# Kernel tuning notes

Measured on AMD Instinct MI355X. Metric: run time of the kernel, lower is better.

Reference implementation:

```python
import jax, jax.numpy as jnp
import numpy as np

DEPTH = 4
HEADS = 8
WINDOW = 256
RPW = 2                      # relay_tokens_per_window
SEQ_PER_RELAY = WINDOW // RPW  # 128 tokens per relay group
RELAY_START = 2              # depth_start_relay_attn (1-indexed layer number)
LN_EPS = 1e-5


def setup_inputs() -> dict:
    key = jax.random.key(0)
    ks = jax.random.split(key, 8)
    b, t, d, dff = 2, 2048, 512, 2048
    s = 0.02
    return {
        "x": jax.random.normal(ks[0], (b, t, d), dtype=jnp.float32),
        "relay_emb": jax.random.normal(ks[1], (1, d), dtype=jnp.float32) * s,
        "ln1_g": jnp.ones((DEPTH, d), jnp.float32),
        "ln1_b": jnp.zeros((DEPTH, d), jnp.float32),
        "loc_qkv_w": jax.random.normal(ks[2], (DEPTH, d, 3 * d), dtype=jnp.float32) * s,
        "loc_out_w": jax.random.normal(ks[3], (DEPTH, d, d), dtype=jnp.float32) * s,
        "loc_out_b": jnp.zeros((DEPTH, d), jnp.float32),
        "glob_qkv_w": jax.random.normal(ks[4], (DEPTH, d, 3 * d), dtype=jnp.float32) * s,
        "glob_out_w": jax.random.normal(ks[5], (DEPTH, d, d), dtype=jnp.float32) * s,
        "glob_out_b": jnp.zeros((DEPTH, d), jnp.float32),
        "ln2_g": jnp.ones((DEPTH, d), jnp.float32),
        "ln2_b": jnp.zeros((DEPTH, d), jnp.float32),
        "ff_w1": jax.random.normal(ks[6], (DEPTH, d, dff), dtype=jnp.float32) * s,
        "ff_b1": jnp.zeros((DEPTH, dff), jnp.float32),
        "ff_w2": jax.random.normal(ks[7], (DEPTH, dff, d), dtype=jnp.float32) * s,
        "ff_b2": jnp.zeros((DEPTH, d), jnp.float32),
    }


def _layernorm(x, g, b):
    m = jnp.mean(x, axis=-1, keepdims=True)
    v = jnp.mean(jnp.square(x - m), axis=-1, keepdims=True)
    return (x - m) * jax.lax.rsqrt(v + LN_EPS) * g + b


def _self_attention(x, qkv_w, out_w, out_b):
    # full (non-causal) multi-head attention, as in FullAttention
    b, t, d = x.shape
    h, dh = HEADS, d // HEADS
    q, k, v = jnp.split(x @ qkv_w, 3, axis=-1)
    mh = lambda u: u.reshape(b, t, h, dh).transpose(0, 2, 1, 3)  # b h t dh
    q, k, v = mh(q), mh(k), mh(v)
    dots = jnp.einsum('bhid,bhjd->bhij', q, k) * (dh ** -0.5)
    attn = jax.nn.softmax(dots, axis=-1)
    o = jnp.einsum('bhij,bhjd->bhid', attn, v)
    o = o.transpose(0, 2, 1, 3).reshape(b, t, d)
    return o @ out_w + out_b


def reference(x, relay_emb, ln1_g, ln1_b, loc_qkv_w, loc_out_w, loc_out_b,
              glob_qkv_w, glob_out_w, glob_out_b, ln2_g, ln2_b,
              ff_w1, ff_b1, ff_w2, ff_b2):
    b, t, d = x.shape
    # insert one relay token every SEQ_PER_RELAY tokens
    x = x.reshape(b, -1, SEQ_PER_RELAY, d)
    G = x.shape[1]
    rel = jnp.broadcast_to(relay_emb[None, None], (b, G, 1, d))
    x = jnp.concatenate([rel, x], axis=2).reshape(b, -1, d)  # (b, G*(129), d)

    for l in range(DEPTH):
        # attention block: PreNorm -> AttentionLayer, residual from sequence wrapper
        y = _layernorm(x, ln1_g[l], ln1_b[l])
        if (l + 1) >= RELAY_START:
            y = y.reshape(b, G, SEQ_PER_RELAY + 1, d)
            r = y[:, :, 0]                                       # (b, G, d) relay tokens
            r = _self_attention(r, glob_qkv_w[l], glob_out_w[l], glob_out_b[l]) + r
            y = jnp.concatenate([r[:, :, None], y[:, :, 1:]], axis=2).reshape(b, -1, d)
        x = x + _self_attention(y, loc_qkv_w[l], loc_out_w[l], loc_out_b[l])
        # feedforward block: PreNorm -> FFN with LeakyReLU(0.01)
        z = _layernorm(x, ln2_g[l], ln2_b[l])
        z = jax.nn.leaky_relu(z @ ff_w1[l] + ff_b1[l], negative_slope=0.01) @ ff_w2[l] + ff_b2[l]
        x = x + z

    # strip relay tokens
    x = x.reshape(b, G, SEQ_PER_RELAY + 1, d)
    return x[:, :, 1:].reshape(b, -1, d)
```

## Files before the change

kernel.cpp:

```cpp
#include <hip/hip_runtime.h>

typedef __attribute__((ext_vector_type(8))) __bf16 bf16x8;
typedef __attribute__((ext_vector_type(8))) unsigned short u16x8;
typedef __attribute__((ext_vector_type(4))) unsigned short u16x4;
typedef __attribute__((ext_vector_type(4))) float f32x4;
typedef unsigned short u16;

#define TSEQ 2064
#define NTOK 4128
#define MPAD 4224

__device__ __forceinline__ float bf2f(u16 u) {
  unsigned x = ((unsigned)u) << 16;
  return __builtin_bit_cast(float, x);
}
__device__ __forceinline__ u16 f2bf(float f) {
  unsigned u = __builtin_bit_cast(unsigned, f);
  u += 0x7fffu + ((u >> 16) & 1u);
  return (u16)(u >> 16);
}

__device__ __forceinline__ void gll16(const u16* g, u16* l) {
  __builtin_amdgcn_global_load_lds((const __attribute__((address_space(1))) void*)g,
                                   (__attribute__((address_space(3))) void*)l, 16, 0, 0);
}
__device__ __forceinline__ int swz(int row, int col) {
  return row * 64 + (col ^ ((row & 7) << 3));
}

__global__ __launch_bounds__(256) void transpose_w(const float* __restrict__ src,
                                                   u16* __restrict__ dst,
                                                   int K, int N)
{
  __shared__ float tile[32][33];
  const int l = blockIdx.z;
  src += (size_t)l * K * N;
  dst += (size_t)l * K * N;
  const int n0 = blockIdx.x * 32, k0 = blockIdx.y * 32;
  const int c = threadIdx.x & 31, r = threadIdx.x >> 5;
#pragma unroll
  for (int rr = r; rr < 32; rr += 8)
    tile[rr][c] = src[(size_t)(k0 + rr) * N + n0 + c];
  __syncthreads();
#pragma unroll
  for (int rr = r; rr < 32; rr += 8)
    dst[(size_t)(n0 + rr) * K + k0 + c] = f2bf(tile[c][rr]);
}

__global__ void build_x(const float* __restrict__ xin, const float* __restrict__ relay,
                        float* __restrict__ xw)
{
  const int total = 2 * TSEQ * 512;
  for (int idx = blockIdx.x * 256 + threadIdx.x; idx < total; idx += gridDim.x * 256) {
    int col = idx & 511;
    int tok = (idx >> 9) % TSEQ;
    int b   = idx / (TSEQ * 512);
    int g = tok / 129, s = tok % 129;
    float v = (s == 0) ? relay[col]
                       : xin[((size_t)b * 2048 + g * 128 + (s - 1)) * 512 + col];
    xw[idx] = v;
  }
}

__global__ void extract_out(const float* __restrict__ xw, float* __restrict__ out)
{
  const int total = 2 * 2048 * 512;
  for (int idx = blockIdx.x * 256 + threadIdx.x; idx < total; idx += gridDim.x * 256) {
    int col = idx & 511;
    int tok = (idx >> 9) & 2047;
    int b   = idx / (2048 * 512);
    int g = tok >> 7, s = tok & 127;
    out[idx] = xw[((size_t)b * TSEQ + g * 129 + s + 1) * 512 + col];
  }
}

__global__ __launch_bounds__(256) void ln_kernel(const float* __restrict__ x,
                                                 const float* __restrict__ g,
                                                 const float* __restrict__ bta,
                                                 u16* __restrict__ y, int M)
{
  const int wid = threadIdx.x >> 6, lane = threadIdx.x & 63;
  const int row = blockIdx.x * 4 + wid;
  if (row >= M) return;
  const float* xr = x + (size_t)row * 512;
  float v[8];
  float s = 0.f;
#pragma unroll
  for (int j = 0; j < 8; ++j) { v[j] = xr[j * 64 + lane]; s += v[j]; }
#pragma unroll
  for (int m = 1; m <= 32; m <<= 1) s += __shfl_xor(s, m);
  float mean = s * (1.f / 512.f);
  float vs = 0.f;
#pragma unroll
  for (int j = 0; j < 8; ++j) { float d = v[j] - mean; vs += d * d; }
#pragma unroll
  for (int m = 1; m <= 32; m <<= 1) vs += __shfl_xor(vs, m);
  float rstd = rsqrtf(vs * (1.f / 512.f) + 1e-5f);
  u16* yr = y + (size_t)row * 512;
#pragma unroll
  for (int j = 0; j < 8; ++j) {
    int c = j * 64 + lane;
    yr[c] = f2bf((v[j] - mean) * rstd * g[c] + bta[c]);
  }
}

template<bool HAS_BIAS, bool ACT, bool RESID, bool OUT_BF16, bool VOUT>
__global__ __launch_bounds__(256) void gemm2(
    const u16* __restrict__ A, const u16* __restrict__ Bt,
    const float* __restrict__ bias, const float* __restrict__ resid,
    void* __restrict__ outp, u16* __restrict__ vgout, int M, int N, int K)
{
  __shared__ __attribute__((aligned(16))) u16 As[2][128 * 64];
  __shared__ __attribute__((aligned(16))) u16 Bs[2][128 * 64];
  const int tid = threadIdx.x, lane = tid & 63, wid = tid >> 6;
  const int row0 = blockIdx.x * 128, col0 = blockIdx.y * 128;
  const int wm = (wid >> 1) * 64, wn = (wid & 1) * 64;
  const int srow = tid >> 3, sseg = tid & 7;
  f32x4 acc[4][4];
#pragma unroll
  for (int m = 0; m < 4; ++m)
#pragma unroll
    for (int n = 0; n < 4; ++n) acc[m][n] = (f32x4)0.f;
  const u16* Ab = A + (size_t)row0 * K;
  const u16* Bb = Bt + (size_t)col0 * K;
#pragma unroll
  for (int i = 0; i < 4; ++i) {
    int row = srow + i * 32, ss = sseg ^ (row & 7);
    gll16(Ab + (size_t)row * K + ss * 8, &As[0][row * 64 + sseg * 8]);
    gll16(Bb + (size_t)row * K + ss * 8, &Bs[0][row * 64 + sseg * 8]);
  }
  const int fr = lane & 15, g = lane >> 4;
  int cur = 0;
  for (int k0 = 0; k0 < K; k0 += 64) {
    __syncthreads();
    if (k0 + 64 < K) {
      u16* ad = &As[cur ^ 1][0];
      u16* bd = &Bs[cur ^ 1][0];
#pragma unroll
      for (int i = 0; i < 4; ++i) {
        int row = srow + i * 32, ss = sseg ^ (row & 7);
        gll16(Ab + (size_t)row * K + k0 + 64 + ss * 8, ad + row * 64 + sseg * 8);
        gll16(Bb + (size_t)row * K + k0 + 64 + ss * 8, bd + row * 64 + sseg * 8);
      }
    }
    const u16* as_ = &As[cur][0];
    const u16* bs_ = &Bs[cur][0];
    bf16x8 a[2][4], bb[2][4];
#pragma unroll
    for (int kk = 0; kk < 2; ++kk) {
#pragma unroll
      for (int m = 0; m < 4; ++m) a[kk][m] = *(const bf16x8*)&as_[swz(wm + m * 16 + fr, kk * 32 + g * 8)];
#pragma unroll
      for (int n = 0; n < 4; ++n) bb[kk][n] = *(const bf16x8*)&bs_[swz(wn + n * 16 + fr, kk * 32 + g * 8)];
    }
    __builtin_amdgcn_s_setprio(1);
#pragma unroll
    for (int kk = 0; kk < 2; ++kk)
#pragma unroll
      for (int m = 0; m < 4; ++m)
#pragma unroll
        for (int n = 0; n < 4; ++n)
          acc[m][n] = __builtin_amdgcn_mfma_f32_16x16x32_bf16(a[kk][m], bb[kk][n], acc[m][n], 0, 0, 0);
    __builtin_amdgcn_s_setprio(0);
    cur ^= 1;
  }

#pragma unroll
  for (int m = 0; m < 4; ++m) {
#pragma unroll
    for (int n = 0; n < 4; ++n) {
#pragma unroll
      for (int j = 0; j < 4; ++j) {
        int grow = row0 + wm + m * 16 + g * 4 + j;
        int gcol = col0 + wn + n * 16 + fr;
        if (grow < M) {
          float v = acc[m][n][j];
          if (HAS_BIAS) v += bias[gcol];
          if (ACT) v = (v > 0.f) ? v : 0.01f * v;
          if (RESID) v += resid[(size_t)grow * N + gcol];
          if (VOUT && gcol >= 1024) {
            int hh = (gcol - 1024) >> 6, dd = gcol & 63;
            int bb2 = grow >= TSEQ;
            int tok = grow - bb2 * TSEQ;
            vgout[((size_t)((bb2 * 8 + hh) * 64 + dd)) * 2112 + tok] = f2bf(v);
          } else if (OUT_BF16) {
            ((u16*)outp)[(size_t)grow * N + gcol] = f2bf(v);
          } else {
            ((float*)outp)[(size_t)grow * N + gcol] = v;
          }
        }
      }
    }
  }
}

__global__ __launch_bounds__(256) void flash_attn3(const u16* __restrict__ big,
                                                   const u16* __restrict__ vg,
                                                   u16* __restrict__ op0,
                                                   u16* __restrict__ op1,
                                                   float2* __restrict__ mlb)
{
  __shared__ __attribute__((aligned(16))) u16 Qs[64 * 64];
  __shared__ __attribute__((aligned(16))) u16 Ks[2][64 * 64];
  __shared__ __attribute__((aligned(16))) u16 Vs[2][64 * 64];
  const int tid = threadIdx.x, lane = tid & 63, wid = tid >> 6;
  const int qt = blockIdx.x, bh = blockIdx.y, z = blockIdx.z;
  const int b = bh >> 3, h = bh & 7;
  const int q0 = qt * 64;
  const int srow = tid >> 3, sseg = tid & 7;
  const int ktbeg = z * 17, ktend = z ? 33 : 17;

  const u16* qb = big + ((size_t)(b * TSEQ) + q0) * 1536 + h * 64;
  const u16* kb = big + ((size_t)(b * TSEQ)) * 1536 + h * 64 + 512;
  const u16* vb = vg + (size_t)bh * 64 * 2112;
#pragma unroll
  for (int i = 0; i < 2; ++i) {
    int row = srow + i * 32, ss = sseg ^ (row & 7);
    gll16(qb + (size_t)row * 1536 + ss * 8, &Qs[row * 64 + sseg * 8]);
    gll16(kb + (size_t)(ktbeg * 64 + row) * 1536 + ss * 8, &Ks[0][row * 64 + sseg * 8]);
    gll16(vb + (size_t)row * 2112 + ktbeg * 64 + ss * 8, &Vs[0][row * 64 + sseg * 8]);
  }
  __syncthreads();
  const int fr = lane & 15, g = lane >> 4;
  bf16x8 aq0 = *(const bf16x8*)&Qs[swz(wid * 16 + fr, g * 8)];
  bf16x8 aq1 = *(const bf16x8*)&Qs[swz(wid * 16 + fr, 32 + g * 8)];
  u16* Pw = &Qs[wid * 1024];

  f32x4 oacc[4];
#pragma unroll
  for (int nf = 0; nf < 4; ++nf) oacc[nf] = (f32x4)0.f;
  float mrow = -1e30f, lsum = 0.f;
  int cur = 0;

  for (int kt = ktbeg; kt < ktend; ++kt) {
    if (kt + 1 < ktend) {
      const u16* kb2 = kb + (size_t)(kt + 1) * 64 * 1536;
      const u16* vb2 = vb + (kt + 1) * 64;
      u16* kd = &Ks[cur ^ 1][0];
      u16* vd = &Vs[cur ^ 1][0];
#pragma unroll
      for (int i = 0; i < 2; ++i) {
        int row = srow + i * 32, ss = sseg ^ (row & 7);
        gll16(kb2 + (size_t)row * 1536 + ss * 8, kd + row * 64 + sseg * 8);
        gll16(vb2 + (size_t)row * 2112 + ss * 8, vd + row * 64 + sseg * 8);
      }
    }
    const u16* ks = &Ks[cur][0];
    const u16* vs = &Vs[cur][0];
    f32x4 s[4];
    __builtin_amdgcn_s_setprio(1);
#pragma unroll
    for (int n = 0; n < 4; ++n) {
      int row = n * 16 + fr;
      bf16x8 ak0 = *(const bf16x8*)&ks[swz(row, g * 8)];
      bf16x8 ak1 = *(const bf16x8*)&ks[swz(row, 32 + g * 8)];
      f32x4 t = (f32x4)0.f;
      t = __builtin_amdgcn_mfma_f32_16x16x32_bf16(ak0, aq0, t, 0, 0, 0);
      t = __builtin_amdgcn_mfma_f32_16x16x32_bf16(ak1, aq1, t, 0, 0, 0);
      s[n] = t;
    }
    __builtin_amdgcn_s_setprio(0);
#pragma unroll
    for (int n = 0; n < 4; ++n) {
      int kbase = kt * 64 + n * 16 + g * 4;
#pragma unroll
      for (int j = 0; j < 4; ++j)
        s[n][j] = (kbase + j < TSEQ) ? s[n][j] * 0.125f : -1e30f;
    }
    float mloc = s[0][0];
#pragma unroll
    for (int n = 0; n < 4; ++n)
#pragma unroll
      for (int j = 0; j < 4; ++j) mloc = fmaxf(mloc, s[n][j]);
    mloc = fmaxf(mloc, __shfl_xor(mloc, 16));
    mloc = fmaxf(mloc, __shfl_xor(mloc, 32));
    float nm = fmaxf(mrow, mloc);
    float sc = __expf(mrow - nm);
    mrow = nm;
    lsum *= sc;
    float psum = 0.f;
#pragma unroll
    for (int n = 0; n < 4; ++n) {
      u16x4 pw;
#pragma unroll
      for (int j = 0; j < 4; ++j) {
        float p = __expf(s[n][j] - nm);
        psum += p;
        pw[j] = f2bf(p);
      }
      *(u16x4*)&Pw[swz(fr, n * 16 + g * 4)] = pw;
    }
    psum += __shfl_xor(psum, 16);
    psum += __shfl_xor(psum, 32);
    lsum += psum;
    float s4[4];
#pragma unroll
    for (int j = 0; j < 4; ++j) s4[j] = __shfl(sc, g * 4 + j);
#pragma unroll
    for (int nf = 0; nf < 4; ++nf)
#pragma unroll
      for (int j = 0; j < 4; ++j) oacc[nf][j] *= s4[j];
    __builtin_amdgcn_s_setprio(1);
#pragma unroll
    for (int kc = 0; kc < 2; ++kc) {
      bf16x8 ap = *(const bf16x8*)&Pw[swz(fr, kc * 32 + g * 8)];
#pragma unroll
      for (int nf = 0; nf < 4; ++nf) {
        bf16x8 bv = *(const bf16x8*)&vs[swz(nf * 16 + fr, kc * 32 + g * 8)];
        oacc[nf] = __builtin_amdgcn_mfma_f32_16x16x32_bf16(ap, bv, oacc[nf], 0, 0, 0);
      }
    }
    __builtin_amdgcn_s_setprio(0);
    __syncthreads();
    cur ^= 1;
  }

  u16* op = z ? op1 : op0;
#pragma unroll
  for (int nf = 0; nf < 4; ++nf) {
#pragma unroll
    for (int j = 0; j < 4; ++j) {
      int row = q0 + wid * 16 + g * 4 + j;
      if (row < TSEQ)
        op[((size_t)(b * TSEQ + row)) * 512 + h * 64 + nf * 16 + fr] = f2bf(oacc[nf][j]);
    }
  }
  if (lane < 16) {
    int row = q0 + wid * 16 + fr;
    if (row < TSEQ)
      mlb[(size_t)(z * 16 + bh) * 2112 + row] = float2{mrow, lsum};
  }
}

__global__ __launch_bounds__(256) void fa_combine(const u16* __restrict__ op0,
                                                  const u16* __restrict__ op1,
                                                  const float2* __restrict__ mlb,
                                                  u16* __restrict__ ob)
{
  int idx = blockIdx.x * 256 + threadIdx.x;
  int tok = idx >> 7;
  int c4 = (idx & 127) * 4;
  int b = tok >= TSEQ;
  int row = tok - b * TSEQ;
  int h = c4 >> 6;
  float2 ml0 = mlb[(size_t)(b * 8 + h) * 2112 + row];
  float2 ml1 = mlb[(size_t)(16 + b * 8 + h) * 2112 + row];
  float M = fmaxf(ml0.x, ml1.x);
  float a0 = __expf(ml0.x - M), a1 = __expf(ml1.x - M);
  float inv = 1.f / (ml0.y * a0 + ml1.y * a1);
  u16x4 v0 = *(const u16x4*)&op0[(size_t)tok * 512 + c4];
  u16x4 v1 = *(const u16x4*)&op1[(size_t)tok * 512 + c4];
  u16x4 o;
#pragma unroll
  for (int j = 0; j < 4; ++j)
    o[j] = f2bf((bf2f(v0[j]) * a0 + bf2f(v1[j]) * a1) * inv);
  *(u16x4*)&ob[(size_t)tok * 512 + c4] = o;
}

__global__ __launch_bounds__(256) void global_attn(const u16* __restrict__ rqkv,
                                                   u16* __restrict__ ro)
{
  const int b = blockIdx.x >> 3, h = blockIdx.x & 7;
  __shared__ float q[16][64], k[16][64], v[16][64], s[16][16], p[16][16];
  const int tid = threadIdx.x;
  for (int idx = tid; idx < 1024; idx += 256) {
    int rr = idx >> 6, c = idx & 63;
    size_t base = (size_t)(b * 16 + rr) * 1536 + h * 64 + c;
    q[rr][c] = bf2f(rqkv[base]);
    k[rr][c] = bf2f(rqkv[base + 512]);
    v[rr][c] = bf2f(rqkv[base + 1024]);
  }
  __syncthreads();
  {
    int i = tid >> 4, j = tid & 15;
    float acc = 0.f;
#pragma unroll
    for (int d = 0; d < 64; ++d) acc += q[i][d] * k[j][d];
    s[i][j] = acc * 0.125f;
  }
  __syncthreads();
  if (tid < 16) {
    float mx = -1e30f;
#pragma unroll
    for (int j = 0; j < 16; ++j) mx = fmaxf(mx, s[tid][j]);
    float sum = 0.f;
#pragma unroll
    for (int j = 0; j < 16; ++j) { float e = __expf(s[tid][j] - mx); p[tid][j] = e; sum += e; }
    float iv = 1.f / sum;
#pragma unroll
    for (int j = 0; j < 16; ++j) p[tid][j] *= iv;
  }
  __syncthreads();
  for (int idx = tid; idx < 1024; idx += 256) {
    int rr = idx >> 6, c = idx & 63;
    float acc = 0.f;
#pragma unroll
    for (int j = 0; j < 16; ++j) acc += p[rr][j] * v[j][c];
    ro[(size_t)(b * 16 + rr) * 512 + h * 64 + c] = f2bf(acc);
  }
}

__global__ void gather_relay(const u16* __restrict__ y, u16* __restrict__ rbuf)
{
  int idx = blockIdx.x * 256 + threadIdx.x;
  int col = idx & 511, rr = idx >> 9;
  int b = rr >> 4, g = rr & 15;
  rbuf[idx] = y[((size_t)b * TSEQ + g * 129) * 512 + col];
}

__global__ void relay_scatter(const float* __restrict__ rout, const u16* __restrict__ rbuf,
                              u16* __restrict__ y)
{
  int idx = blockIdx.x * 256 + threadIdx.x;
  int col = idx & 511, rr = idx >> 9;
  int b = rr >> 4, g = rr & 15;
  y[((size_t)b * TSEQ + g * 129) * 512 + col] = f2bf(rout[idx] + bf2f(rbuf[idx]));
}

extern "C" void kernel_launch(void* const* d_in, const int* in_sizes, int n_in,
                              void* d_out, int out_size, void* d_ws, size_t ws_size,
                              hipStream_t stream)
{
  const float* x_in     = (const float*)d_in[0];
  const float* rel_emb  = (const float*)d_in[1];
  const float* ln1_g    = (const float*)d_in[2];
  const float* ln1_b    = (const float*)d_in[3];
  const float* loc_qkv  = (const float*)d_in[4];
  const float* loc_ow   = (const float*)d_in[5];
  const float* loc_ob   = (const float*)d_in[6];
  const float* glob_qkv = (const float*)d_in[7];
  const float* glob_ow  = (const float*)d_in[8];
  const float* glob_ob  = (const float*)d_in[9];
  const float* ln2_g    = (const float*)d_in[10];
  const float* ln2_b    = (const float*)d_in[11];
  const float* ff_w1    = (const float*)d_in[12];
  const float* ff_b1    = (const float*)d_in[13];
  const float* ff_w2    = (const float*)d_in[14];
  const float* ff_b2    = (const float*)d_in[15];

  char* ws = (char*)d_ws;
  float* xbuf = (float*)(ws + 0);
  u16*   ybuf = (u16*)(ws + 8650752);
  u16*   obuf = (u16*)(ws + 12976128);
  u16*   big  = (u16*)(ws + 17301504);
  u16*   vg   = (u16*)(ws + 34603008);
  u16*   wLQ  = (u16*)(ws + 38928384);
  u16*   wGQ  = (u16*)(ws + 45219840);
  u16*   wLO  = (u16*)(ws + 51511296);
  u16*   wGO  = (u16*)(ws + 53608448);
  u16*   wF1  = (u16*)(ws + 55705600);
  u16*   wF2  = (u16*)(ws + 64094208);
  u16*   rbuf = (u16*)(ws + 72482816);
  u16*   rqkv = (u16*)(ws + 72613888);
  u16*   rov  = (u16*)(ws + 72712192);
  float* rout = (float*)(ws + 72843264);
  float2* mlb = (float2*)(ws + 72908800);

  dim3 B(256);
  transpose_w<<<dim3(48, 16, 4), B, 0, stream>>>(loc_qkv, wLQ, 512, 1536);
  transpose_w<<<dim3(48, 16, 4), B, 0, stream>>>(glob_qkv, wGQ, 512, 1536);
  transpose_w<<<dim3(16, 16, 4), B, 0, stream>>>(loc_ow, wLO, 512, 512);
  transpose_w<<<dim3(16, 16, 4), B, 0, stream>>>(glob_ow, wGO, 512, 512);
  transpose_w<<<dim3(64, 16, 4), B, 0, stream>>>(ff_w1, wF1, 512, 2048);
  transpose_w<<<dim3(16, 64, 4), B, 0, stream>>>(ff_w2, wF2, 2048, 512);

  build_x<<<8256, B, 0, stream>>>(x_in, rel_emb, xbuf);

  for (int l = 0; l < 4; ++l) {
    ln_kernel<<<1032, B, 0, stream>>>(xbuf, ln1_g + l * 512, ln1_b + l * 512, ybuf, NTOK);
    if (l + 1 >= 2) {
      gather_relay<<<64, B, 0, stream>>>(ybuf, rbuf);
      gemm2<false, false, false, true, false><<<dim3(1, 12), B, 0, stream>>>(
          rbuf, wGQ + (size_t)l * 1536 * 512, nullptr, nullptr, rqkv, nullptr, 32, 1536, 512);
      global_attn<<<16, B, 0, stream>>>(rqkv, rov);
      gemm2<true, false, false, false, false><<<dim3(1, 4), B, 0, stream>>>(
          rov, wGO + (size_t)l * 512 * 512, glob_ob + l * 512, nullptr, rout, nullptr, 32, 512, 512);
      relay_scatter<<<64, B, 0, stream>>>(rout, rbuf, ybuf);
    }
    gemm2<false, false, false, true, true><<<dim3(33, 12), B, 0, stream>>>(
        ybuf, wLQ + (size_t)l * 1536 * 512, nullptr, nullptr, big, vg, NTOK, 1536, 512);
    flash_attn3<<<dim3(33, 16, 2), B, 0, stream>>>(big, vg, ybuf, obuf, mlb);
    fa_combine<<<2064, B, 0, stream>>>(ybuf, obuf, mlb, obuf);
    gemm2<true, false, true, false, false><<<dim3(33, 4), B, 0, stream>>>(
        obuf, wLO + (size_t)l * 512 * 512, loc_ob + l * 512, xbuf, xbuf, nullptr, NTOK, 512, 512);
    ln_kernel<<<1032, B, 0, stream>>>(xbuf, ln2_g + l * 512, ln2_b + l * 512, ybuf, NTOK);
    gemm2<true, true, false, true, false><<<dim3(33, 16), B, 0, stream>>>(
        ybuf, wF1 + (size_t)l * 2048 * 512, ff_b1 + l * 2048, nullptr, big, nullptr, NTOK, 2048, 512);
    gemm2<true, false, true, false, false><<<dim3(33, 4), B, 0, stream>>>(
        big, wF2 + (size_t)l * 512 * 2048, ff_b2 + l * 512, xbuf, xbuf, nullptr, NTOK, 512, 2048);
  }
  extract_out<<<8192, B, 0, stream>>>(xbuf, (float*)d_out);
}
```

Measured before the change: 1.071 ms.

## Fuse relay gather/scatter into GEMM, single-buffer GEMM, 128-row flash attention with lazy rescale

The six weight-transpose launches are merged into one kernel, and the relay gather/scatter kernels are folded into the GEMM's A-row indexing and epilogue. The GEMM drops double-buffered LDS for a single buffer with an occupancy hint, which trades load/compute overlap for more resident blocks. Flash attention now uses 512-thread blocks covering 128 query rows. The softmax scale is pre-applied to Q in the QKV GEMM epilogue, masking runs only on the last tile, and the running-max rescale is skipped while the max stays within a threshold. P is packed to bf16 by truncation rather than round-to-nearest, which slightly changes numerics.

```diff
diff --git a/kernel.cpp b/kernel.cpp
--- a/kernel.cpp
+++ b/kernel.cpp
@@ -3,12 +3,13 @@
 typedef __attribute__((ext_vector_type(8))) __bf16 bf16x8;
 typedef __attribute__((ext_vector_type(8))) unsigned short u16x8;
 typedef __attribute__((ext_vector_type(4))) unsigned short u16x4;
+typedef __attribute__((ext_vector_type(2))) unsigned int u32x2;
 typedef __attribute__((ext_vector_type(4))) float f32x4;
 typedef unsigned short u16;
+typedef unsigned int u32;
 
 #define TSEQ 2064
 #define NTOK 4128
-#define MPAD 4224
 
 __device__ __forceinline__ float bf2f(u16 u) {
   unsigned x = ((unsigned)u) << 16;
@@ -28,22 +29,34 @@
   return row * 64 + (col ^ ((row & 7) << 3));
 }
 
-__global__ __launch_bounds__(256) void transpose_w(const float* __restrict__ src,
-                                                   u16* __restrict__ dst,
-                                                   int K, int N)
+__global__ __launch_bounds__(256) void transpose_all(
+    const float* __restrict__ s0, const float* __restrict__ s1,
+    const float* __restrict__ s2, const float* __restrict__ s3,
+    const float* __restrict__ s4, const float* __restrict__ s5,
+    u16* __restrict__ d0, u16* __restrict__ d1, u16* __restrict__ d2,
+    u16* __restrict__ d3, u16* __restrict__ d4, u16* __restrict__ d5)
 {
   __shared__ float tile[32][33];
-  const int l = blockIdx.z;
+  int bid = blockIdx.x;
+  const float* src; u16* dst; int K, N, r;
+  if (bid < 6144)       { int w = bid >> 11 >= 1 && bid >= 3072; r = bid - (bid >= 3072 ? 3072 : 0);
+                          K = 512; N = 1536; src = bid >= 3072 ? s1 : s0; dst = bid >= 3072 ? d1 : d0; }
+  else if (bid < 8192)  { r = bid - (bid >= 7168 ? 7168 : 6144);
+                          K = 512; N = 512;  src = bid >= 7168 ? s3 : s2; dst = bid >= 7168 ? d3 : d2; }
+  else if (bid < 12288) { r = bid - 8192;  K = 512;  N = 2048; src = s4; dst = d4; }
+  else                  { r = bid - 12288; K = 2048; N = 512;  src = s5; dst = d5; }
+  const int tx = N >> 5, per = tx * (K >> 5);
+  const int l = r / per; r -= l * per;
+  const int n0 = (r % tx) * 32, k0 = (r / tx) * 32;
   src += (size_t)l * K * N;
   dst += (size_t)l * K * N;
-  const int n0 = blockIdx.x * 32, k0 = blockIdx.y * 32;
-  const int c = threadIdx.x & 31, r = threadIdx.x >> 5;
-#pragma unroll
-  for (int rr = r; rr < 32; rr += 8)
+  const int c = threadIdx.x & 31, rr0 = threadIdx.x >> 5;
+#pragma unroll
+  for (int rr = rr0; rr < 32; rr += 8)
     tile[rr][c] = src[(size_t)(k0 + rr) * N + n0 + c];
   __syncthreads();
 #pragma unroll
-  for (int rr = r; rr < 32; rr += 8)
+  for (int rr = rr0; rr < 32; rr += 8)
     dst[(size_t)(n0 + rr) * K + k0 + c] = f2bf(tile[c][rr]);
 }
 
@@ -104,14 +117,19 @@
   }
 }
 
-template<bool HAS_BIAS, bool ACT, bool RESID, bool OUT_BF16, bool VOUT>
-__global__ __launch_bounds__(256) void gemm2(
+__device__ __forceinline__ int relay_tok(int r) {
+  return (r >> 4) * TSEQ + (r & 15) * 129;
+}
+
+template<bool HAS_BIAS, bool ACT, bool RESID, bool OUT_BF16, bool VOUT,
+         bool RELAYA, bool RELAYC>
+__global__ __launch_bounds__(256, 4) void gemm3(
     const u16* __restrict__ A, const u16* __restrict__ Bt,
     const float* __restrict__ bias, const float* __restrict__ resid,
     void* __restrict__ outp, u16* __restrict__ vgout, int M, int N, int K)
 {
-  __shared__ __attribute__((aligned(16))) u16 As[2][128 * 64];
-  __shared__ __attribute__((aligned(16))) u16 Bs[2][128 * 64];
+  __shared__ __attribute__((aligned(16))) u16 As[128 * 64];
+  __shared__ __attribute__((aligned(16))) u16 Bs[128 * 64];
   const int tid = threadIdx.x, lane = tid & 63, wid = tid >> 6;
   const int row0 = blockIdx.x * 128, col0 = blockIdx.y * 128;
   const int wm = (wid >> 1) * 64, wn = (wid & 1) * 64;
@@ -121,48 +139,34 @@
   for (int m = 0; m < 4; ++m)
 #pragma unroll
     for (int n = 0; n < 4; ++n) acc[m][n] = (f32x4)0.f;
-  const u16* Ab = A + (size_t)row0 * K;
   const u16* Bb = Bt + (size_t)col0 * K;
-#pragma unroll
-  for (int i = 0; i < 4; ++i) {
-    int row = srow + i * 32, ss = sseg ^ (row & 7);
-    gll16(Ab + (size_t)row * K + ss * 8, &As[0][row * 64 + sseg * 8]);
-    gll16(Bb + (size_t)row * K + ss * 8, &Bs[0][row * 64 + sseg * 8]);
-  }
   const int fr = lane & 15, g = lane >> 4;
-  int cur = 0;
+
   for (int k0 = 0; k0 < K; k0 += 64) {
     __syncthreads();
-    if (k0 + 64 < K) {
-      u16* ad = &As[cur ^ 1][0];
-      u16* bd = &Bs[cur ^ 1][0];
-#pragma unroll
-      for (int i = 0; i < 4; ++i) {
-        int row = srow + i * 32, ss = sseg ^ (row & 7);
-        gll16(Ab + (size_t)row * K + k0 + 64 + ss * 8, ad + row * 64 + sseg * 8);
-        gll16(Bb + (size_t)row * K + k0 + 64 + ss * 8, bd + row * 64 + sseg * 8);
-      }
-    }
-    const u16* as_ = &As[cur][0];
-    const u16* bs_ = &Bs[cur][0];
-    bf16x8 a[2][4], bb[2][4];
+#pragma unroll
+    for (int i = 0; i < 4; ++i) {
+      int row = srow + i * 32, ss = sseg ^ (row & 7);
+      size_t arow = RELAYA ? (size_t)relay_tok(row & 31) : (size_t)(row0 + row);
+      gll16(A + arow * K + k0 + ss * 8, &As[row * 64 + sseg * 8]);
+      gll16(Bb + (size_t)row * K + k0 + ss * 8, &Bs[row * 64 + sseg * 8]);
+    }
+    __syncthreads();
 #pragma unroll
     for (int kk = 0; kk < 2; ++kk) {
-#pragma unroll
-      for (int m = 0; m < 4; ++m) a[kk][m] = *(const bf16x8*)&as_[swz(wm + m * 16 + fr, kk * 32 + g * 8)];
-#pragma unroll
-      for (int n = 0; n < 4; ++n) bb[kk][n] = *(const bf16x8*)&bs_[swz(wn + n * 16 + fr, kk * 32 + g * 8)];
-    }
-    __builtin_amdgcn_s_setprio(1);
-#pragma unroll
-    for (int kk = 0; kk < 2; ++kk)
+      bf16x8 a[4], bb[4];
+#pragma unroll
+      for (int m = 0; m < 4; ++m) a[m] = *(const bf16x8*)&As[swz(wm + m * 16 + fr, kk * 32 + g * 8)];
+#pragma unroll
+      for (int n = 0; n < 4; ++n) bb[n] = *(const bf16x8*)&Bs[swz(wn + n * 16 + fr, kk * 32 + g * 8)];
+      __builtin_amdgcn_s_setprio(1);
 #pragma unroll
       for (int m = 0; m < 4; ++m)
 #pragma unroll
         for (int n = 0; n < 4; ++n)
-          acc[m][n] = __builtin_amdgcn_mfma_f32_16x16x32_bf16(a[kk][m], bb[kk][n], acc[m][n], 0, 0, 0);
-    __builtin_amdgcn_s_setprio(0);
-    cur ^= 1;
+          acc[m][n] = __builtin_amdgcn_mfma_f32_16x16x32_bf16(a[m], bb[n], acc[m][n], 0, 0, 0);
+      __builtin_amdgcn_s_setprio(0);
+    }
   }
 
 #pragma unroll
@@ -178,12 +182,16 @@
           if (HAS_BIAS) v += bias[gcol];
           if (ACT) v = (v > 0.f) ? v : 0.01f * v;
           if (RESID) v += resid[(size_t)grow * N + gcol];
-          if (VOUT && gcol >= 1024) {
+          if (RELAYC) {
+            u16* p = (u16*)outp + (size_t)relay_tok(grow) * 512 + gcol;
+            *p = f2bf(v + bf2f(*p));
+          } else if (VOUT && gcol >= 1024) {
             int hh = (gcol - 1024) >> 6, dd = gcol & 63;
             int bb2 = grow >= TSEQ;
             int tok = grow - bb2 * TSEQ;
             vgout[((size_t)((bb2 * 8 + hh) * 64 + dd)) * 2112 + tok] = f2bf(v);
           } else if (OUT_BF16) {
+            if (VOUT && gcol < 512) v *= 0.125f;
             ((u16*)outp)[(size_t)grow * N + gcol] = f2bf(v);
           } else {
             ((float*)outp)[(size_t)grow * N + gcol] = v;
@@ -194,31 +202,35 @@
   }
 }
 
-__global__ __launch_bounds__(256) void flash_attn3(const u16* __restrict__ big,
-                                                   const u16* __restrict__ vg,
-                                                   u16* __restrict__ op0,
-                                                   u16* __restrict__ op1,
-                                                   float2* __restrict__ mlb)
-{
-  __shared__ __attribute__((aligned(16))) u16 Qs[64 * 64];
+__global__ __launch_bounds__(512, 4) void flash_attn4(const u16* __restrict__ big,
+                                                      const u16* __restrict__ vg,
+                                                      u16* __restrict__ op0,
+                                                      u16* __restrict__ op1,
+                                                      float2* __restrict__ mlb)
+{
+  __shared__ __attribute__((aligned(16))) u16 Qs[128 * 64];
   __shared__ __attribute__((aligned(16))) u16 Ks[2][64 * 64];
   __shared__ __attribute__((aligned(16))) u16 Vs[2][64 * 64];
   const int tid = threadIdx.x, lane = tid & 63, wid = tid >> 6;
   const int qt = blockIdx.x, bh = blockIdx.y, z = blockIdx.z;
   const int b = bh >> 3, h = bh & 7;
-  const int q0 = qt * 64;
+  const int q0 = qt * 128;
   const int srow = tid >> 3, sseg = tid & 7;
   const int ktbeg = z * 17, ktend = z ? 33 : 17;
 
-  const u16* qb = big + ((size_t)(b * TSEQ) + q0) * 1536 + h * 64;
   const u16* kb = big + ((size_t)(b * TSEQ)) * 1536 + h * 64 + 512;
   const u16* vb = vg + (size_t)bh * 64 * 2112;
 #pragma unroll
   for (int i = 0; i < 2; ++i) {
-    int row = srow + i * 32, ss = sseg ^ (row & 7);
-    gll16(qb + (size_t)row * 1536 + ss * 8, &Qs[row * 64 + sseg * 8]);
-    gll16(kb + (size_t)(ktbeg * 64 + row) * 1536 + ss * 8, &Ks[0][row * 64 + sseg * 8]);
-    gll16(vb + (size_t)row * 2112 + ktbeg * 64 + ss * 8, &Vs[0][row * 64 + sseg * 8]);
+    int row = srow + i * 64;
+    int grow = b * TSEQ + q0 + row; grow = grow < NTOK ? grow : NTOK - 1;
+    int ss = sseg ^ (row & 7);
+    gll16(big + (size_t)grow * 1536 + h * 64 + ss * 8, &Qs[row * 64 + sseg * 8]);
+  }
+  {
+    int ss = sseg ^ (srow & 7);
+    gll16(kb + (size_t)(ktbeg * 64 + srow) * 1536 + ss * 8, &Ks[0][srow * 64 + sseg * 8]);
+    gll16(vb + (size_t)srow * 2112 + ktbeg * 64 + ss * 8, &Vs[0][srow * 64 + sseg * 8]);
   }
   __syncthreads();
   const int fr = lane & 15, g = lane >> 4;
@@ -234,16 +246,9 @@
 
   for (int kt = ktbeg; kt < ktend; ++kt) {
     if (kt + 1 < ktend) {
-      const u16* kb2 = kb + (size_t)(kt + 1) * 64 * 1536;
-      const u16* vb2 = vb + (kt + 1) * 64;
-      u16* kd = &Ks[cur ^ 1][0];
-      u16* vd = &Vs[cur ^ 1][0];
-#pragma unroll
-      for (int i = 0; i < 2; ++i) {
-        int row = srow + i * 32, ss = sseg ^ (row & 7);
-        gll16(kb2 + (size_t)row * 1536 + ss * 8, kd + row * 64 + sseg * 8);
-        gll16(vb2 + (size_t)row * 2112 + ss * 8, vd + row * 64 + sseg * 8);
-      }
+      int ss = sseg ^ (srow & 7);
+      gll16(kb + (size_t)((kt + 1) * 64 + srow) * 1536 + ss * 8, &Ks[cur ^ 1][srow * 64 + sseg * 8]);
+      gll16(vb + (size_t)srow * 2112 + (kt + 1) * 64 + ss * 8, &Vs[cur ^ 1][srow * 64 + sseg * 8]);
     }
     const u16* ks = &Ks[cur][0];
     const u16* vs = &Vs[cur][0];
@@ -260,12 +265,14 @@
       s[n] = t;
     }
     __builtin_amdgcn_s_setprio(0);
-#pragma unroll
-    for (int n = 0; n < 4; ++n) {
-      int kbase = kt * 64 + n * 16 + g * 4;
-#pragma unroll
-      for (int j = 0; j < 4; ++j)
-        s[n][j] = (kbase + j < TSEQ) ? s[n][j] * 0.125f : -1e30f;
+    if (kt == 32) {
+#pragma unroll
+      for (int n = 0; n < 4; ++n) {
+        int kbase = kt * 64 + n * 16 + g * 4;
+#pragma unroll
+        for (int j = 0; j < 4; ++j)
+          if (kbase + j >= TSEQ) s[n][j] = -1e30f;
+      }
     }
     float mloc = s[0][0];
 #pragma unroll
@@ -274,32 +281,33 @@
       for (int j = 0; j < 4; ++j) mloc = fmaxf(mloc, s[n][j]);
     mloc = fmaxf(mloc, __shfl_xor(mloc, 16));
     mloc = fmaxf(mloc, __shfl_xor(mloc, 32));
-    float nm = fmaxf(mrow, mloc);
-    float sc = __expf(mrow - nm);
-    mrow = nm;
-    lsum *= sc;
+    if (!__all(mloc <= mrow + 8.f)) {
+      float nm = fmaxf(mrow, mloc);
+      float sc = __expf(mrow - nm);
+      mrow = nm;
+      lsum *= sc;
+      float s4[4];
+#pragma unroll
+      for (int j = 0; j < 4; ++j) s4[j] = __shfl(sc, g * 4 + j);
+#pragma unroll
+      for (int nf = 0; nf < 4; ++nf)
+#pragma unroll
+        for (int j = 0; j < 4; ++j) oacc[nf][j] *= s4[j];
+    }
     float psum = 0.f;
 #pragma unroll
     for (int n = 0; n < 4; ++n) {
-      u16x4 pw;
-#pragma unroll
-      for (int j = 0; j < 4; ++j) {
-        float p = __expf(s[n][j] - nm);
-        psum += p;
-        pw[j] = f2bf(p);
-      }
-      *(u16x4*)&Pw[swz(fr, n * 16 + g * 4)] = pw;
+      float p0 = __expf(s[n][0] - mrow), p1 = __expf(s[n][1] - mrow);
+      float p2 = __expf(s[n][2] - mrow), p3 = __expf(s[n][3] - mrow);
+      psum += (p0 + p1) + (p2 + p3);
+      u32x2 pk;
+      pk[0] = __builtin_amdgcn_perm(__builtin_bit_cast(u32, p1), __builtin_bit_cast(u32, p0), 0x07060302u);
+      pk[1] = __builtin_amdgcn_perm(__builtin_bit_cast(u32, p3), __builtin_bit_cast(u32, p2), 0x07060302u);
+      *(u32x2*)&Pw[swz(fr, n * 16 + g * 4)] = pk;
     }
     psum += __shfl_xor(psum, 16);
     psum += __shfl_xor(psum, 32);
     lsum += psum;
-    float s4[4];
-#pragma unroll
-    for (int j = 0; j < 4; ++j) s4[j] = __shfl(sc, g * 4 + j);
-#pragma unroll
-    for (int nf = 0; nf < 4; ++nf)
-#pragma unroll
-      for (int j = 0; j < 4; ++j) oacc[nf][j] *= s4[j];
     __builtin_amdgcn_s_setprio(1);
 #pragma unroll
     for (int kc = 0; kc < 2; ++kc) {
@@ -398,23 +406,6 @@
     for (int j = 0; j < 16; ++j) acc += p[rr][j] * v[j][c];
     ro[(size_t)(b * 16 + rr) * 512 + h * 64 + c] = f2bf(acc);
   }
-}
-
-__global__ void gather_relay(const u16* __restrict__ y, u16* __restrict__ rbuf)
-{
-  int idx = blockIdx.x * 256 + threadIdx.x;
-  int col = idx & 511, rr = idx >> 9;
-  int b = rr >> 4, g = rr & 15;
-  rbuf[idx] = y[((size_t)b * TSEQ + g * 129) * 512 + col];
-}
-
-__global__ void relay_scatter(const float* __restrict__ rout, const u16* __restrict__ rbuf,
-                              u16* __restrict__ y)
-{
-  int idx = blockIdx.x * 256 + threadIdx.x;
-  int col = idx & 511, rr = idx >> 9;
-  int b = rr >> 4, g = rr & 15;
-  y[((size_t)b * TSEQ + g * 129) * 512 + col] = f2bf(rout[idx] + bf2f(rbuf[idx]));
 }
 
 extern "C" void kernel_launch(void* const* d_in, const int* in_sizes, int n_in,
@@ -439,54 +430,45 @@
   const float* ff_b2    = (const float*)d_in[15];
 
   char* ws = (char*)d_ws;
-  float* xbuf = (float*)(ws + 0);
-  u16*   ybuf = (u16*)(ws + 8650752);
-  u16*   obuf = (u16*)(ws + 12976128);
-  u16*   big  = (u16*)(ws + 17301504);
-  u16*   vg   = (u16*)(ws + 34603008);
-  u16*   wLQ  = (u16*)(ws + 38928384);
-  u16*   wGQ  = (u16*)(ws + 45219840);
-  u16*   wLO  = (u16*)(ws + 51511296);
-  u16*   wGO  = (u16*)(ws + 53608448);
-  u16*   wF1  = (u16*)(ws + 55705600);
-  u16*   wF2  = (u16*)(ws + 64094208);
-  u16*   rbuf = (u16*)(ws + 72482816);
-  u16*   rqkv = (u16*)(ws + 72613888);
-  u16*   rov  = (u16*)(ws + 72712192);
-  float* rout = (float*)(ws + 72843264);
-  float2* mlb = (float2*)(ws + 72908800);
+  float*  xbuf = (float*)(ws + 0);
+  u16*    ybuf = (u16*)(ws + 8650752);
+  u16*    obuf = (u16*)(ws + 12976128);
+  u16*    big  = (u16*)(ws + 17301504);
+  u16*    vg   = (u16*)(ws + 34603008);
+  u16*    wLQ  = (u16*)(ws + 38928384);
+  u16*    wGQ  = (u16*)(ws + 45219840);
+  u16*    wLO  = (u16*)(ws + 51511296);
+  u16*    wGO  = (u16*)(ws + 53608448);
+  u16*    wF1  = (u16*)(ws + 55705600);
+  u16*    wF2  = (u16*)(ws + 64094208);
+  u16*    rqkv = (u16*)(ws + 72482816);
+  u16*    rov  = (u16*)(ws + 72581120);
+  float2* mlb  = (float2*)(ws + 72712192);
 
   dim3 B(256);
-  transpose_w<<<dim3(48, 16, 4), B, 0, stream>>>(loc_qkv, wLQ, 512, 1536);
-  transpose_w<<<dim3(48, 16, 4), B, 0, stream>>>(glob_qkv, wGQ, 512, 1536);
-  transpose_w<<<dim3(16, 16, 4), B, 0, stream>>>(loc_ow, wLO, 512, 512);
-  transpose_w<<<dim3(16, 16, 4), B, 0, stream>>>(glob_ow, wGO, 512, 512);
-  transpose_w<<<dim3(64, 16, 4), B, 0, stream>>>(ff_w1, wF1, 512, 2048);
-  transpose_w<<<dim3(16, 64, 4), B, 0, stream>>>(ff_w2, wF2, 2048, 512);
-
+  transpose_all<<<16384, B, 0, stream>>>(loc_qkv, glob_qkv, loc_ow, glob_ow, ff_w1, ff_w2,
+                                         wLQ, wGQ, wLO, wGO, wF1, wF2);
   build_x<<<8256, B, 0, stream>>>(x_in, rel_emb, xbuf);
 
   for (int l = 0; l < 4; ++l) {
     ln_kernel<<<1032, B, 0, stream>>>(xbuf, ln1_g + l * 512, ln1_b + l * 512, ybuf, NTOK);
     if (l + 1 >= 2) {
-      gather_relay<<<64, B, 0, stream>>>(ybuf, rbuf);
-      gemm2<false, false, false, true, false><<<dim3(1, 12), B, 0, stream>>>(
-          rbuf, wGQ + (size_t)l * 1536 * 512, nullptr, nullptr, rqkv, nullptr, 32, 1536, 512);
+      gemm3<false, false, false, true, false, true, false><<<dim3(1, 12), B, 0, stream>>>(
+          ybuf, wGQ + (size_t)l * 1536 * 512, nullptr, nullptr, rqkv, nullptr, 32, 1536, 512);
       global_attn<<<16, B, 0, stream>>>(rqkv, rov);
-      gemm2<true, false, false, false, false><<<dim3(1, 4), B, 0, stream>>>(
-          rov, wGO + (size_t)l * 512 * 512, glob_ob + l * 512, nullptr, rout, nullptr, 32, 512, 512);
-      relay_scatter<<<64, B, 0, stream>>>(rout, rbuf, ybuf);
-    }
-    gemm2<false, false, false, true, true><<<dim3(33, 12), B, 0, stream>>>(
+      gemm3<true, false, false, true, false, false, true><<<dim3(1, 4), B, 0, stream>>>(
+          rov, wGO + (size_t)l * 512 * 512, glob_ob + l * 512, nullptr, ybuf, nullptr, 32, 512, 512);
+    }
+    gemm3<false, false, false, true, true, false, false><<<dim3(33, 12), B, 0, stream>>>(
         ybuf, wLQ + (size_t)l * 1536 * 512, nullptr, nullptr, big, vg, NTOK, 1536, 512);
-    flash_attn3<<<dim3(33, 16, 2), B, 0, stream>>>(big, vg, ybuf, obuf, mlb);
+    flash_attn4<<<dim3(17, 16, 2), dim3(512), 0, stream>>>(big, vg, ybuf, obuf, mlb);
     fa_combine<<<2064, B, 0, stream>>>(ybuf, obuf, mlb, obuf);
-    gemm2<true, false, true, false, false><<<dim3(33, 4), B, 0, stream>>>(
+    gemm3<true, false, true, false, false, false, false><<<dim3(33, 4), B, 0, stream>>>(
         obuf, wLO + (size_t)l * 512 * 512, loc_ob + l * 512, xbuf, xbuf, nullptr, NTOK, 512, 512);
     ln_kernel<<<1032, B, 0, stream>>>(xbuf, ln2_g + l * 512, ln2_b + l * 512, ybuf, NTOK);
-    gemm2<true, true, false, true, false><<<dim3(33, 16), B, 0, stream>>>(
+    gemm3<true, true, false, true, false, false, false><<<dim3(33, 16), B, 0, stream>>>(
         ybuf, wF1 + (size_t)l * 2048 * 512, ff_b1 + l * 2048, nullptr, big, nullptr, NTOK, 2048, 512);
-    gemm2<true, false, true, false, false><<<dim3(33, 4), B, 0, stream>>>(
+    gemm3<true, false, true, false, false, false, false><<<dim3(33, 4), B, 0, stream>>>(
         big, wF2 + (size_t)l * 512 * 2048, ff_b2 + l * 512, xbuf, xbuf, nullptr, NTOK, 512, 2048);
   }
   extract_out<<<8192, B, 0, stream>>>(xbuf, (float*)d_out);
```

Result: faster. 931.9 us (-13.0%).
